# Kernel tuning notes

Measured on AMD Instinct MI355X. Metric: run time of the kernel, lower is better.

The kernel has to match this reference:

```python
import jax, jax.numpy as jnp
import numpy as np

BETA = 100.0
# (in_ch, out_ch) for the 12 effective 1x1-conv layers. ResNeXt blocks are
# fused: all branches read the same block input, so stacking branch weights
# along out-channels gives one GEMM per block.
LAYER_DIMS = [(259, 515), (515, 512), (512, 512), (512, 576), (576, 576),
              (576, 768), (768, 768), (768, 768), (768, 960), (960, 960),
              (960, 896), (896, 1)]


def setup_inputs() -> dict:
    key = jax.random.key(0)
    keys = jax.random.split(key, 2 + len(LAYER_DIMS))
    B, N = 2, 8192
    inp = {
        "input": jax.random.normal(keys[0], (B, N, 3), dtype=jnp.float32),
        "latent": jax.random.normal(keys[1], (B, 256), dtype=jnp.float32),
    }
    for i, (cin, cout) in enumerate(LAYER_DIMS):
        std = np.sqrt(2.0) / np.sqrt(cin)
        inp[f"W{i+1}"] = std * jax.random.normal(keys[2 + i], (cout, cin), dtype=jnp.float32)
        inp[f"b{i+1}"] = jnp.zeros((cout,), dtype=jnp.float32)
    return inp


def _sp(z):
    # torch Softplus(beta=100): softplus(beta*z)/beta (jax.nn.softplus is stable)
    return jax.nn.softplus(BETA * z) / BETA


def reference(input, latent,
              W1, b1, W2, b2, W3, b3, W4, b4, W5, b5, W6, b6,
              W7, b7, W8, b8, W9, b9, W10, b10, W11, b11, W12, b12):
    B, N, _ = input.shape
    lat = jnp.broadcast_to(latent[:, None, :], (B, N, latent.shape[-1]))
    x = jnp.concatenate([input, lat], axis=-1)  # (B, N, 259)
    input_con = x

    # layer 1: conv + softplus, grad seeded from first 3 input columns (xyz)
    z = x @ W1.T + b1                                   # (B, N, 515)
    g = jax.nn.sigmoid(BETA * z)[..., None] * W1[:, :3]  # (B, N, 515, 3)
    x = _sp(z)

    mids = [(W2, b2), (W3, b3), (W4, b4), (W5, b5), (W6, b6), (W7, b7),
            (W8, b8), (W9, b9), (W10, b10), (W11, b11)]
    for W, b in mids:  # fixed small layer loop (10 fused ResNeXt blocks)
        z = x @ W.T + b                                 # (B, N, Cout)
        g = jax.nn.sigmoid(BETA * z)[..., None] * jnp.einsum('oc,bnci->bnoi', W, g)
        x = _sp(z)

    # final 1x1 conv, no activation
    z = x @ W12.T + b12                                 # (B, N, 1)
    g = jnp.einsum('oc,bnci->bnoi', W12, g)             # (B, N, 1, 3)
    # torch returns conv output channel-first: (B, 1, N)
    return (z.transpose(0, 2, 1), g, input_con)
```

## Files before the change

### kernel.cpp

```cpp
#include <hip/hip_runtime.h>
#include <math.h>


typedef unsigned short u16;
typedef _Float16 f16;
typedef f16   f16x8  __attribute__((ext_vector_type(8)));
typedef float f32x16 __attribute__((ext_vector_type(16)));

__device__ __forceinline__ u16   f2h(float x){ return __builtin_bit_cast(u16, (f16)x); }
__device__ __forceinline__ float h2f(u16 b){ return (float)__builtin_bit_cast(f16, b); }

__device__ __forceinline__ void glld16(const void* g, void* l){
  __builtin_amdgcn_global_load_lds(
      (const __attribute__((address_space(1))) unsigned*)g,
      (__attribute__((address_space(3))) unsigned*)l, 16, 0, 0);
}

template<int N> __device__ __forceinline__ void wait_vmcnt(){
  static_assert(N == 0 || N == 6 || N == 9, "unsupported vmcnt literal");
  if constexpr (N == 0) asm volatile("s_waitcnt vmcnt(0)" ::: "memory");
  if constexpr (N == 6) asm volatile("s_waitcnt vmcnt(6)" ::: "memory");
  if constexpr (N == 9) asm volatile("s_waitcnt vmcnt(9)" ::: "memory");
}

template<int NP>
__global__ __launch_bounds__(256, 2)
void fused_layer(const u16* __restrict__ Sin, long long psIn, int kpad,
                 u16* __restrict__ Sout, long long psOut, int opitch,
                 const u16* __restrict__ Wh, const u16* __restrict__ Wl,
                 const float* __restrict__ bias, const float* __restrict__ Wfirst,
                 int cout, int cinFirst)
{
  constexpr bool FIRST = (NP == 2);
  constexpr int  S     = NP + 4;
  __shared__ u16 As[2][NP][4][64][8];
  __shared__ u16 Bs[2][2][4][128][8];

  int bx = blockIdx.x, by = blockIdx.y;
  {
    const int gx = gridDim.x, gy = gridDim.y;
    const int nwg = gx * gy;
    const int d   = by * gx + bx;
    if ((nwg & 7) == 0){
      const int q = nwg >> 3;
      const int t = (d & 7) * q + (d >> 3);
      by = t % gy;
      bx = t / gy;
    }
  }

  const int tid   = threadIdx.x;
  const int w     = tid >> 6;
  const int lane  = tid & 63;
  const int lrow  = lane & 31;
  const int lhalf = lane >> 5;
  const int mh    = w >> 1;
  const int oh    = w & 1;
  const int m0    = bx * 64;
  const int o0    = by * 128;

  f32x16 zinit = {};
  f32x16 accx[2];
  f32x16 accg[FIRST ? 1 : 3][2];
  accx[0] = zinit; accx[1] = zinit;
  if constexpr (!FIRST){
    #pragma unroll
    for (int j = 0; j < 3; ++j){ accg[j][0] = zinit; accg[j][1] = zinit; }
  }

  const u16* aSrc[NP];
  #pragma unroll
  for (int p = 0; p < NP; ++p)
    aSrc[p] = Sin + (long long)p * psIn + (long long)(m0 + lane) * kpad + w * 8;
  const u16* bSrc[2][2];
  #pragma unroll
  for (int h = 0; h < 2; ++h){
    const u16* Wx = h ? Wl : Wh;
    #pragma unroll
    for (int hf = 0; hf < 2; ++hf)
      bSrc[h][hf] = Wx + (long long)(o0 + hf*64 + lane) * kpad + w * 8;
  }

  auto stage = [&](int buf, int kElem){
    #pragma unroll
    for (int p = 0; p < NP; ++p)
      glld16(aSrc[p] + kElem, &As[buf][p][w][0][0]);
    #pragma unroll
    for (int h = 0; h < 2; ++h)
      #pragma unroll
      for (int hf = 0; hf < 2; ++hf)
        glld16(bSrc[h][hf] + kElem, &Bs[buf][h][w][hf*64][0]);
  };

  auto compute = [&](int buf){
    __builtin_amdgcn_s_setprio(1);
    #pragma unroll
    for (int s = 0; s < 2; ++s){
      const int kq = s*2 + lhalf;
      f16x8 a[NP];
      #pragma unroll
      for (int p = 0; p < NP; ++p)
        a[p] = *(const f16x8*)&As[buf][p][kq][mh*32 + lrow][0];
      #pragma unroll
      for (int f = 0; f < 2; ++f){
        const int oc = oh*64 + f*32 + lrow;
        f16x8 bh = *(const f16x8*)&Bs[buf][0][kq][oc][0];
        f16x8 bl = *(const f16x8*)&Bs[buf][1][kq][oc][0];
        accx[f] = __builtin_amdgcn_mfma_f32_32x32x16_f16(a[0], bh, accx[f], 0,0,0);
        accx[f] = __builtin_amdgcn_mfma_f32_32x32x16_f16(a[1], bh, accx[f], 0,0,0);
        accx[f] = __builtin_amdgcn_mfma_f32_32x32x16_f16(a[0], bl, accx[f], 0,0,0);
        if constexpr (!FIRST){
          #pragma unroll
          for (int j = 0; j < 3; ++j)
            accg[j][f] = __builtin_amdgcn_mfma_f32_32x32x16_f16(a[2+j], bh, accg[j][f], 0,0,0);
        }
      }
    }
    __builtin_amdgcn_s_setprio(0);
  };

  const int nk = kpad >> 5;
  stage(0, 0);
  stage(1, 32);
  int cur = 0;
  for (int t = 0; t < nk - 1; ++t){
    wait_vmcnt<S>();
    __builtin_amdgcn_s_barrier();
    compute(cur);
    asm volatile("s_waitcnt lgkmcnt(0)" ::: "memory");
    __builtin_amdgcn_s_barrier();
    if (t + 2 < nk) stage(cur, (t + 2) * 32);
    cur ^= 1;
  }
  wait_vmcnt<0>();
  __builtin_amdgcn_s_barrier();
  compute(cur);

  const int mb = m0 + mh*32;
  #pragma unroll
  for (int f = 0; f < 2; ++f){
    const int o = o0 + oh*64 + f*32 + lrow;
    if (o >= opitch) continue;
    const float bo = (o < cout) ? bias[o] : 0.f;
    float w0 = 0.f, w1 = 0.f, w2 = 0.f;
    if constexpr (FIRST){
      if (o < cout){
        w0 = Wfirst[(long long)o*cinFirst + 0];
        w1 = Wfirst[(long long)o*cinFirst + 1];
        w2 = Wfirst[(long long)o*cinFirst + 2];
      }
    }
    #pragma unroll
    for (int r = 0; r < 16; ++r){
      const int m = mb + (r & 3) + ((r >> 2) << 3) + (lhalf << 2);
      const float z    = accx[f][r] + bo;
      const float gate = 1.f / (1.f + expf(-100.f * z));
      const float sp   = fmaxf(z, 0.f) + 0.01f * log1pf(expf(-100.f * fabsf(z)));
      const long long idx = (long long)m * opitch + o;
      const u16 xh = f2h(sp);
      Sout[idx]          = xh;
      Sout[psOut + idx]  = f2h(sp - h2f(xh));
      if constexpr (FIRST){
        Sout[2*psOut + idx] = f2h(gate * w0);
        Sout[3*psOut + idx] = f2h(gate * w1);
        Sout[4*psOut + idx] = f2h(gate * w2);
      } else {
        Sout[2*psOut + idx] = f2h(gate * accg[0][f][r]);
        Sout[3*psOut + idx] = f2h(gate * accg[1][f][r]);
        Sout[4*psOut + idx] = f2h(gate * accg[2][f][r]);
      }
    }
  }
}

__global__ __launch_bounds__(256)
void final_layer(const u16* __restrict__ Sin, long long ps, int kpad,
                 const float* __restrict__ W, const float* __restrict__ bias,
                 float* __restrict__ out1, float* __restrict__ out2,
                 int cin, int mBase)
{
  const int lane = threadIdx.x & 63;
  const int wv   = threadIdx.x >> 6;
  const int m = blockIdx.x * 4 + wv;
  const u16* row = Sin + (long long)m * kpad;
  float s0=0.f, s1=0.f, s2=0.f, s3=0.f;
  for (int c = lane; c < cin; c += 64){
    const float w = W[c];
    s0 += (h2f(row[c]) + h2f(row[ps + c])) * w;
    s1 += h2f(row[2*ps + c]) * w;
    s2 += h2f(row[3*ps + c]) * w;
    s3 += h2f(row[4*ps + c]) * w;
  }
  #pragma unroll
  for (int off = 32; off > 0; off >>= 1){
    s0 += __shfl_xor(s0, off); s1 += __shfl_xor(s1, off);
    s2 += __shfl_xor(s2, off); s3 += __shfl_xor(s3, off);
  }
  if (lane == 0){
    out1[mBase + m] = s0 + bias[0];
    float* g = out2 + (long long)(mBase + m) * 3;
    g[0] = s1; g[1] = s2; g[2] = s3;
  }
}

__global__ void prep_input(const float* __restrict__ input,
                           const float* __restrict__ latent,
                           float* __restrict__ out3,
                           u16* __restrict__ x0, long long psX0, int N)
{
  const int m = blockIdx.x;
  const int b = m / N;
  const int c = threadIdx.x;
  if (c >= 288) return;
  float v = 0.f;
  if (c < 3) v = input[(long long)m*3 + c];
  else if (c < 259) v = latent[(long long)b*256 + (c - 3)];
  if (c < 259) out3[(long long)m*259 + c] = v;
  const u16 h = f2h(v);
  x0[(long long)m*288 + c]        = h;
  x0[psX0 + (long long)m*288 + c] = f2h(v - h2f(h));
}

__global__ void split_w(const float* __restrict__ W, u16* __restrict__ wh,
                        u16* __restrict__ wl, int cout, int cin, int kpad, int total)
{
  const int idx = blockIdx.x * 256 + threadIdx.x;
  if (idx >= total) return;
  const int o = idx / kpad, c = idx % kpad;
  const float v = (o < cout && c < cin) ? W[(long long)o*cin + c] : 0.f;
  const u16 h = f2h(v);
  wh[idx] = h;
  wl[idx] = f2h(v - h2f(h));
}

extern "C" void kernel_launch(void* const* d_in, const int* in_sizes, int n_in,
                              void* d_out, int out_size, void* d_ws, size_t ws_size,
                              hipStream_t stream)
{
  static const int CIN [12] = {259,515,512,512,576,576,768,768,768,960,960,896};
  static const int COUT[12] = {515,512,512,576,576,768,768,768,960,960,896,1};
  int NY[11], ROWS[11], KPAD[12];
  KPAD[0] = 288;
  for (int i = 0; i < 11; ++i){
    NY[i]    = (COUT[i] + 127) / 128;
    ROWS[i]  = NY[i] * 128;
    KPAD[i+1] = (COUT[i] + 31) & ~31;
  }

  const float* input  = (const float*)d_in[0];
  const float* latent = (const float*)d_in[1];
  auto Wp = [&](int i){ return (const float*)d_in[2 + 2*i]; };
  auto Bp = [&](int i){ return (const float*)d_in[3 + 2*i]; };

  const int Bn = in_sizes[1] / 256;
  const int Nn = in_sizes[0] / (3 * Bn);
  const int M  = Bn * Nn;

  float* out1 = (float*)d_out;
  float* out2 = out1 + M;
  float* out3 = out2 + (size_t)M * 3;

  char* wsp = (char*)d_ws;
  u16 *WH[11], *WL[11];
  for (int i = 0; i < 11; ++i){
    const size_t sz = (size_t)ROWS[i] * KPAD[i] * 2;
    WH[i] = (u16*)wsp; wsp += sz;
    WL[i] = (u16*)wsp; wsp += sz;
  }
  u16* x0 = (u16*)wsp;
  const long long psX0 = (long long)M * 288;
  wsp += (size_t)2 * psX0 * 2;

  const size_t used = (size_t)(wsp - (char*)d_ws);
  const size_t remain = (ws_size > used) ? (ws_size - used) : 0;
  const size_t perPoint = (size_t)2 * 5 * 960 * 2;
  long long pc = (long long)(remain / perPoint);
  pc &= ~63LL;
  int Pc = (int)((pc < (long long)M) ? pc : (long long)M);
  if (Pc < 64) Pc = 64;
  u16* bufA = (u16*)wsp;
  u16* bufB = bufA + (size_t)5 * Pc * 960;

  prep_input<<<M, 320, 0, stream>>>(input, latent, out3, x0, psX0, Nn);
  for (int i = 0; i < 11; ++i){
    const int total = ROWS[i] * KPAD[i];
    split_w<<<(total + 255)/256, 256, 0, stream>>>(
        Wp(i), WH[i], WL[i], COUT[i], CIN[i], KPAD[i], total);
  }

  for (int cm0 = 0; cm0 < M; cm0 += Pc){
    const int Mc = (M - cm0 < Pc) ? (M - cm0) : Pc;

    {
      dim3 g(Mc/64, NY[0]);
      fused_layer<2><<<g, 256, 0, stream>>>(
          x0 + (long long)cm0 * 288, psX0, 288,
          bufA, (long long)Pc * KPAD[1], KPAD[1],
          WH[0], WL[0], Bp(0), Wp(0), COUT[0], CIN[0]);
    }
    u16* src = bufA;
    u16* dst = bufB;
    for (int i = 1; i <= 10; ++i){
      dim3 g(Mc/64, NY[i]);
      fused_layer<5><<<g, 256, 0, stream>>>(
          src, (long long)Pc * KPAD[i], KPAD[i],
          dst, (long long)Pc * KPAD[i+1], KPAD[i+1],
          WH[i], WL[i], Bp(i), nullptr, COUT[i], 0);
      u16* t = src; src = dst; dst = t;
    }
    final_layer<<<Mc/4, 256, 0, stream>>>(
        src, (long long)Pc * KPAD[11], KPAD[11],
        Wp(11), Bp(11), out1, out2, CIN[11], cm0);
  }
}
```

Measured before the change: 2.646 ms.

## Replace forward-mode Jacobian propagation with stored gates and reverse-mode backward GEMMs

Forward-mode carried three gradient planes through every layer, adding three extra MFMA chains and three extra output planes per layer. The new version stores only each layer's sigmoid gate during the forward pass and then runs a reverse (vector-Jacobian) pass. That pass starts from W12 and multiplies by transposed weights, one plane per layer, and a final kernel contracts the result with W1[:, :3]. This removes about half the GEMM work but adds ten backward GEMM launches and keeps all eleven gate tensors in workspace, which can shrink the point chunk size.

Measured after the change: 2.705 ms. 1.02x slower.

```diff
diff --git a/kernel.cpp b/kernel.cpp
--- a/kernel.cpp
+++ b/kernel.cpp
@@ -17,37 +17,38 @@
 }
 
 template<int N> __device__ __forceinline__ void wait_vmcnt(){
-  static_assert(N == 0 || N == 6 || N == 9, "unsupported vmcnt literal");
+  static_assert(N == 0 || N == 3 || N == 6, "unsupported vmcnt literal");
   if constexpr (N == 0) asm volatile("s_waitcnt vmcnt(0)" ::: "memory");
+  if constexpr (N == 3) asm volatile("s_waitcnt vmcnt(3)" ::: "memory");
   if constexpr (N == 6) asm volatile("s_waitcnt vmcnt(6)" ::: "memory");
-  if constexpr (N == 9) asm volatile("s_waitcnt vmcnt(9)" ::: "memory");
-}
-
-template<int NP>
-__global__ __launch_bounds__(256, 2)
-void fused_layer(const u16* __restrict__ Sin, long long psIn, int kpad,
-                 u16* __restrict__ Sout, long long psOut, int opitch,
-                 const u16* __restrict__ Wh, const u16* __restrict__ Wl,
-                 const float* __restrict__ bias, const float* __restrict__ Wfirst,
-                 int cout, int cinFirst)
-{
-  constexpr bool FIRST = (NP == 2);
-  constexpr int  S     = NP + 4;
-  __shared__ u16 As[2][NP][4][64][8];
+}
+
+__device__ __forceinline__ void xcd_map(int& bx, int& by){
+  const int gx = gridDim.x, gy = gridDim.y;
+  const int nwg = gx * gy;
+  const int d   = by * gx + bx;
+  if ((nwg & 7) == 0){
+    const int q = nwg >> 3;
+    const int t = (d & 7) * q + (d >> 3);
+    by = t % gy;
+    bx = t / gy;
+  }
+}
+
+template<bool LAST>
+__global__ __launch_bounds__(256, 3)
+void fwd_layer(const u16* __restrict__ Sin, long long psIn, int kpad,
+               u16* __restrict__ SoutX, long long psOut,
+               u16* __restrict__ Gout, int opitch,
+               const u16* __restrict__ Wh, const u16* __restrict__ Wl,
+               const float* __restrict__ bias, const float* __restrict__ w12,
+               int cout)
+{
+  __shared__ u16 As[2][2][4][64][8];
   __shared__ u16 Bs[2][2][4][128][8];
 
   int bx = blockIdx.x, by = blockIdx.y;
-  {
-    const int gx = gridDim.x, gy = gridDim.y;
-    const int nwg = gx * gy;
-    const int d   = by * gx + bx;
-    if ((nwg & 7) == 0){
-      const int q = nwg >> 3;
-      const int t = (d & 7) * q + (d >> 3);
-      by = t % gy;
-      bx = t / gy;
-    }
-  }
+  xcd_map(bx, by);
 
   const int tid   = threadIdx.x;
   const int w     = tid >> 6;
@@ -61,16 +62,11 @@
 
   f32x16 zinit = {};
   f32x16 accx[2];
-  f32x16 accg[FIRST ? 1 : 3][2];
   accx[0] = zinit; accx[1] = zinit;
-  if constexpr (!FIRST){
-    #pragma unroll
-    for (int j = 0; j < 3; ++j){ accg[j][0] = zinit; accg[j][1] = zinit; }
-  }
-
-  const u16* aSrc[NP];
-  #pragma unroll
-  for (int p = 0; p < NP; ++p)
+
+  const u16* aSrc[2];
+  #pragma unroll
+  for (int p = 0; p < 2; ++p)
     aSrc[p] = Sin + (long long)p * psIn + (long long)(m0 + lane) * kpad + w * 8;
   const u16* bSrc[2][2];
   #pragma unroll
@@ -83,7 +79,7 @@
 
   auto stage = [&](int buf, int kElem){
     #pragma unroll
-    for (int p = 0; p < NP; ++p)
+    for (int p = 0; p < 2; ++p)
       glld16(aSrc[p] + kElem, &As[buf][p][w][0][0]);
     #pragma unroll
     for (int h = 0; h < 2; ++h)
@@ -97,23 +93,16 @@
     #pragma unroll
     for (int s = 0; s < 2; ++s){
       const int kq = s*2 + lhalf;
-      f16x8 a[NP];
-      #pragma unroll
-      for (int p = 0; p < NP; ++p)
-        a[p] = *(const f16x8*)&As[buf][p][kq][mh*32 + lrow][0];
+      f16x8 a0 = *(const f16x8*)&As[buf][0][kq][mh*32 + lrow][0];
+      f16x8 a1 = *(const f16x8*)&As[buf][1][kq][mh*32 + lrow][0];
       #pragma unroll
       for (int f = 0; f < 2; ++f){
         const int oc = oh*64 + f*32 + lrow;
         f16x8 bh = *(const f16x8*)&Bs[buf][0][kq][oc][0];
         f16x8 bl = *(const f16x8*)&Bs[buf][1][kq][oc][0];
-        accx[f] = __builtin_amdgcn_mfma_f32_32x32x16_f16(a[0], bh, accx[f], 0,0,0);
-        accx[f] = __builtin_amdgcn_mfma_f32_32x32x16_f16(a[1], bh, accx[f], 0,0,0);
-        accx[f] = __builtin_amdgcn_mfma_f32_32x32x16_f16(a[0], bl, accx[f], 0,0,0);
-        if constexpr (!FIRST){
-          #pragma unroll
-          for (int j = 0; j < 3; ++j)
-            accg[j][f] = __builtin_amdgcn_mfma_f32_32x32x16_f16(a[2+j], bh, accg[j][f], 0,0,0);
-        }
+        accx[f] = __builtin_amdgcn_mfma_f32_32x32x16_f16(a0, bh, accx[f], 0,0,0);
+        accx[f] = __builtin_amdgcn_mfma_f32_32x32x16_f16(a1, bh, accx[f], 0,0,0);
+        accx[f] = __builtin_amdgcn_mfma_f32_32x32x16_f16(a0, bl, accx[f], 0,0,0);
       }
     }
     __builtin_amdgcn_s_setprio(0);
@@ -124,7 +113,7 @@
   stage(1, 32);
   int cur = 0;
   for (int t = 0; t < nk - 1; ++t){
-    wait_vmcnt<S>();
+    wait_vmcnt<6>();
     __builtin_amdgcn_s_barrier();
     compute(cur);
     asm volatile("s_waitcnt lgkmcnt(0)" ::: "memory");
@@ -141,15 +130,9 @@
   for (int f = 0; f < 2; ++f){
     const int o = o0 + oh*64 + f*32 + lrow;
     if (o >= opitch) continue;
-    const float bo = (o < cout) ? bias[o] : 0.f;
-    float w0 = 0.f, w1 = 0.f, w2 = 0.f;
-    if constexpr (FIRST){
-      if (o < cout){
-        w0 = Wfirst[(long long)o*cinFirst + 0];
-        w1 = Wfirst[(long long)o*cinFirst + 1];
-        w2 = Wfirst[(long long)o*cinFirst + 2];
-      }
-    }
+    const bool real = (o < cout);
+    const float bo  = real ? bias[o] : 0.f;
+    const float wf  = (LAST && real) ? w12[o] : 0.f;
     #pragma unroll
     for (int r = 0; r < 16; ++r){
       const int m = mb + (r & 3) + ((r >> 2) << 3) + (lhalf << 2);
@@ -158,48 +141,140 @@
       const float sp   = fmaxf(z, 0.f) + 0.01f * log1pf(expf(-100.f * fabsf(z)));
       const long long idx = (long long)m * opitch + o;
       const u16 xh = f2h(sp);
-      Sout[idx]          = xh;
-      Sout[psOut + idx]  = f2h(sp - h2f(xh));
-      if constexpr (FIRST){
-        Sout[2*psOut + idx] = f2h(gate * w0);
-        Sout[3*psOut + idx] = f2h(gate * w1);
-        Sout[4*psOut + idx] = f2h(gate * w2);
-      } else {
-        Sout[2*psOut + idx] = f2h(gate * accg[0][f][r]);
-        Sout[3*psOut + idx] = f2h(gate * accg[1][f][r]);
-        Sout[4*psOut + idx] = f2h(gate * accg[2][f][r]);
+      SoutX[idx]         = xh;
+      SoutX[psOut + idx] = f2h(sp - h2f(xh));
+      float gv;
+      if (LAST) gv = gate * wf;
+      else      gv = real ? gate : 0.f;
+      Gout[idx] = f2h(gv);
+    }
+  }
+}
+
+__global__ __launch_bounds__(256, 4)
+void bwd_layer(const u16* __restrict__ Vin, int kpad,
+               u16* __restrict__ Vout, int opitch,
+               const u16* __restrict__ Gprev, const u16* __restrict__ Wt)
+{
+  __shared__ u16 As[2][4][64][8];
+  __shared__ u16 Bs[2][4][128][8];
+
+  int bx = blockIdx.x, by = blockIdx.y;
+  xcd_map(bx, by);
+
+  const int tid   = threadIdx.x;
+  const int w     = tid >> 6;
+  const int lane  = tid & 63;
+  const int lrow  = lane & 31;
+  const int lhalf = lane >> 5;
+  const int mh    = w >> 1;
+  const int oh    = w & 1;
+  const int m0    = bx * 64;
+  const int o0    = by * 128;
+
+  f32x16 zinit = {};
+  f32x16 acc[2];
+  acc[0] = zinit; acc[1] = zinit;
+
+  const u16* aSrc = Vin + (long long)(m0 + lane) * kpad + w * 8;
+  const u16* bSrc[2];
+  #pragma unroll
+  for (int hf = 0; hf < 2; ++hf)
+    bSrc[hf] = Wt + (long long)(o0 + hf*64 + lane) * kpad + w * 8;
+
+  auto stage = [&](int buf, int kElem){
+    glld16(aSrc + kElem, &As[buf][w][0][0]);
+    #pragma unroll
+    for (int hf = 0; hf < 2; ++hf)
+      glld16(bSrc[hf] + kElem, &Bs[buf][w][hf*64][0]);
+  };
+
+  auto compute = [&](int buf){
+    __builtin_amdgcn_s_setprio(1);
+    #pragma unroll
+    for (int s = 0; s < 2; ++s){
+      const int kq = s*2 + lhalf;
+      f16x8 a = *(const f16x8*)&As[buf][kq][mh*32 + lrow][0];
+      #pragma unroll
+      for (int f = 0; f < 2; ++f){
+        const int oc = oh*64 + f*32 + lrow;
+        f16x8 b = *(const f16x8*)&Bs[buf][kq][oc][0];
+        acc[f] = __builtin_amdgcn_mfma_f32_32x32x16_f16(a, b, acc[f], 0,0,0);
       }
     }
+    __builtin_amdgcn_s_setprio(0);
+  };
+
+  const int nk = kpad >> 5;
+  stage(0, 0);
+  stage(1, 32);
+  int cur = 0;
+  for (int t = 0; t < nk - 1; ++t){
+    wait_vmcnt<3>();
+    __builtin_amdgcn_s_barrier();
+    compute(cur);
+    asm volatile("s_waitcnt lgkmcnt(0)" ::: "memory");
+    __builtin_amdgcn_s_barrier();
+    if (t + 2 < nk) stage(cur, (t + 2) * 32);
+    cur ^= 1;
+  }
+  wait_vmcnt<0>();
+  __builtin_amdgcn_s_barrier();
+  compute(cur);
+
+  const int mb = m0 + mh*32;
+  #pragma unroll
+  for (int f = 0; f < 2; ++f){
+    const int o = o0 + oh*64 + f*32 + lrow;
+    if (o >= opitch) continue;
+    #pragma unroll
+    for (int r = 0; r < 16; ++r){
+      const int m = mb + (r & 3) + ((r >> 2) << 3) + (lhalf << 2);
+      const long long idx = (long long)m * opitch + o;
+      Vout[idx] = f2h(acc[f][r] * h2f(Gprev[idx]));
+    }
   }
 }
 
 __global__ __launch_bounds__(256)
-void final_layer(const u16* __restrict__ Sin, long long ps, int kpad,
-                 const float* __restrict__ W, const float* __restrict__ bias,
-                 float* __restrict__ out1, float* __restrict__ out2,
-                 int cin, int mBase)
+void final_z(const u16* __restrict__ Sx, long long ps, int kpad,
+             const float* __restrict__ W12, const float* __restrict__ b12,
+             float* __restrict__ out1, int cin, int mBase)
 {
   const int lane = threadIdx.x & 63;
   const int wv   = threadIdx.x >> 6;
   const int m = blockIdx.x * 4 + wv;
-  const u16* row = Sin + (long long)m * kpad;
-  float s0=0.f, s1=0.f, s2=0.f, s3=0.f;
-  for (int c = lane; c < cin; c += 64){
-    const float w = W[c];
-    s0 += (h2f(row[c]) + h2f(row[ps + c])) * w;
-    s1 += h2f(row[2*ps + c]) * w;
-    s2 += h2f(row[3*ps + c]) * w;
-    s3 += h2f(row[4*ps + c]) * w;
+  const u16* row = Sx + (long long)m * kpad;
+  float s = 0.f;
+  for (int c = lane; c < cin; c += 64)
+    s += (h2f(row[c]) + h2f(row[ps + c])) * W12[c];
+  #pragma unroll
+  for (int off = 32; off > 0; off >>= 1) s += __shfl_xor(s, off);
+  if (lane == 0) out1[mBase + m] = s + b12[0];
+}
+
+__global__ __launch_bounds__(256)
+void final_g(const u16* __restrict__ V0, int kpad,
+             const float* __restrict__ W1, int cinW,
+             float* __restrict__ out2, int width, int mBase)
+{
+  const int lane = threadIdx.x & 63;
+  const int wv   = threadIdx.x >> 6;
+  const int m = blockIdx.x * 4 + wv;
+  const u16* row = V0 + (long long)m * kpad;
+  float g0 = 0.f, g1 = 0.f, g2 = 0.f;
+  for (int o = lane; o < width; o += 64){
+    const float v = h2f(row[o]);
+    const float* wr = W1 + (long long)o * cinW;
+    g0 += v * wr[0]; g1 += v * wr[1]; g2 += v * wr[2];
   }
   #pragma unroll
   for (int off = 32; off > 0; off >>= 1){
-    s0 += __shfl_xor(s0, off); s1 += __shfl_xor(s1, off);
-    s2 += __shfl_xor(s2, off); s3 += __shfl_xor(s3, off);
+    g0 += __shfl_xor(g0, off); g1 += __shfl_xor(g1, off); g2 += __shfl_xor(g2, off);
   }
   if (lane == 0){
-    out1[mBase + m] = s0 + bias[0];
     float* g = out2 + (long long)(mBase + m) * 3;
-    g[0] = s1; g[1] = s2; g[2] = s3;
+    g[0] = g0; g[1] = g1; g[2] = g2;
   }
 }
 
@@ -233,24 +308,34 @@
   wl[idx] = f2h(v - h2f(h));
 }
 
+__global__ void split_wt(const float* __restrict__ W, u16* __restrict__ wt,
+                         int cout, int cin, int kpad, int total)
+{
+  const int idx = blockIdx.x * 256 + threadIdx.x;
+  if (idx >= total) return;
+  const int c = idx / kpad, k = idx % kpad;
+  const float v = (c < cin && k < cout) ? W[(long long)k*cin + c] : 0.f;
+  wt[idx] = f2h(v);
+}
+
 extern "C" void kernel_launch(void* const* d_in, const int* in_sizes, int n_in,
                               void* d_out, int out_size, void* d_ws, size_t ws_size,
                               hipStream_t stream)
 {
   static const int CIN [12] = {259,515,512,512,576,576,768,768,768,960,960,896};
   static const int COUT[12] = {515,512,512,576,576,768,768,768,960,960,896,1};
-  int NY[11], ROWS[11], KPAD[12];
-  KPAD[0] = 288;
-  for (int i = 0; i < 11; ++i){
-    NY[i]    = (COUT[i] + 127) / 128;
-    ROWS[i]  = NY[i] * 128;
-    KPAD[i+1] = (COUT[i] + 31) & ~31;
+  int PF[11], KPF[11], NYF[11], NYB[11];
+  for (int j = 0; j < 11; ++j){
+    PF[j]  = (COUT[j] + 31) & ~31;
+    KPF[j] = (j == 0) ? 288 : PF[j-1];
+    NYF[j] = (COUT[j] + 127) / 128;
+    NYB[j] = (CIN[j] + 127) / 128;
   }
 
   const float* input  = (const float*)d_in[0];
   const float* latent = (const float*)d_in[1];
-  auto Wp = [&](int i){ return (const float*)d_in[2 + 2*i]; };
-  auto Bp = [&](int i){ return (const float*)d_in[3 + 2*i]; };
+  auto Wp = [&](int j){ return (const float*)d_in[2 + 2*j]; };
+  auto Bp = [&](int j){ return (const float*)d_in[3 + 2*j]; };
 
   const int Bn = in_sizes[1] / 256;
   const int Nn = in_sizes[0] / (3 * Bn);
@@ -261,55 +346,86 @@
   float* out3 = out2 + (size_t)M * 3;
 
   char* wsp = (char*)d_ws;
-  u16 *WH[11], *WL[11];
-  for (int i = 0; i < 11; ++i){
-    const size_t sz = (size_t)ROWS[i] * KPAD[i] * 2;
-    WH[i] = (u16*)wsp; wsp += sz;
-    WL[i] = (u16*)wsp; wsp += sz;
+  u16 *WH[11], *WL[11], *WT[11];
+  for (int j = 0; j < 11; ++j){
+    const size_t sz = (size_t)NYF[j] * 128 * KPF[j] * 2;
+    WH[j] = (u16*)wsp; wsp += sz;
+    WL[j] = (u16*)wsp; wsp += sz;
+  }
+  for (int j = 1; j < 11; ++j){
+    const size_t sz = (size_t)NYB[j] * 128 * PF[j] * 2;
+    WT[j] = (u16*)wsp; wsp += sz;
   }
   u16* x0 = (u16*)wsp;
   const long long psX0 = (long long)M * 288;
   wsp += (size_t)2 * psX0 * 2;
 
-  const size_t used = (size_t)(wsp - (char*)d_ws);
+  size_t sumPF = 0;
+  for (int j = 0; j < 11; ++j) sumPF += (size_t)PF[j];
+  const size_t used   = (size_t)(wsp - (char*)d_ws);
   const size_t remain = (ws_size > used) ? (ws_size - used) : 0;
-  const size_t perPoint = (size_t)2 * 5 * 960 * 2;
+  const size_t perPoint = sumPF * 2 + (size_t)2 * 2 * 960 * 2;
   long long pc = (long long)(remain / perPoint);
   pc &= ~63LL;
   int Pc = (int)((pc < (long long)M) ? pc : (long long)M);
   if (Pc < 64) Pc = 64;
+
+  u16* gates[11];
+  for (int j = 0; j < 11; ++j){
+    gates[j] = (u16*)wsp; wsp += (size_t)Pc * PF[j] * 2;
+  }
   u16* bufA = (u16*)wsp;
-  u16* bufB = bufA + (size_t)5 * Pc * 960;
+  u16* bufB = bufA + (size_t)2 * Pc * 960;
+  u16* vA = bufB;
+  u16* vB = bufB + (size_t)Pc * 960;
 
   prep_input<<<M, 320, 0, stream>>>(input, latent, out3, x0, psX0, Nn);
-  for (int i = 0; i < 11; ++i){
-    const int total = ROWS[i] * KPAD[i];
+  for (int j = 0; j < 11; ++j){
+    const int total = NYF[j] * 128 * KPF[j];
     split_w<<<(total + 255)/256, 256, 0, stream>>>(
-        Wp(i), WH[i], WL[i], COUT[i], CIN[i], KPAD[i], total);
+        Wp(j), WH[j], WL[j], COUT[j], CIN[j], KPF[j], total);
+  }
+  for (int j = 1; j < 11; ++j){
+    const int total = NYB[j] * 128 * PF[j];
+    split_wt<<<(total + 255)/256, 256, 0, stream>>>(
+        Wp(j), WT[j], COUT[j], CIN[j], PF[j], total);
   }
 
   for (int cm0 = 0; cm0 < M; cm0 += Pc){
     const int Mc = (M - cm0 < Pc) ? (M - cm0) : Pc;
-
-    {
-      dim3 g(Mc/64, NY[0]);
-      fused_layer<2><<<g, 256, 0, stream>>>(
-          x0 + (long long)cm0 * 288, psX0, 288,
-          bufA, (long long)Pc * KPAD[1], KPAD[1],
-          WH[0], WL[0], Bp(0), Wp(0), COUT[0], CIN[0]);
-    }
-    u16* src = bufA;
-    u16* dst = bufB;
-    for (int i = 1; i <= 10; ++i){
-      dim3 g(Mc/64, NY[i]);
-      fused_layer<5><<<g, 256, 0, stream>>>(
-          src, (long long)Pc * KPAD[i], KPAD[i],
-          dst, (long long)Pc * KPAD[i+1], KPAD[i+1],
-          WH[i], WL[i], Bp(i), nullptr, COUT[i], 0);
-      u16* t = src; src = dst; dst = t;
-    }
-    final_layer<<<Mc/4, 256, 0, stream>>>(
-        src, (long long)Pc * KPAD[11], KPAD[11],
-        Wp(11), Bp(11), out1, out2, CIN[11], cm0);
-  }
-}
+    const int gx = Mc / 64;
+
+    u16* src = x0 + (long long)cm0 * 288;
+    long long psSrc = psX0;
+    int kp = 288;
+    u16* dstTbl[2] = { bufA, bufB };
+    for (int j = 0; j < 11; ++j){
+      u16* dst = dstTbl[j & 1];
+      dim3 g(gx, NYF[j]);
+      if (j == 10)
+        fwd_layer<true><<<g, 256, 0, stream>>>(
+            src, psSrc, kp, dst, (long long)Pc * PF[j], gates[j], PF[j],
+            WH[j], WL[j], Bp(j), Wp(11), COUT[j]);
+      else
+        fwd_layer<false><<<g, 256, 0, stream>>>(
+            src, psSrc, kp, dst, (long long)Pc * PF[j], gates[j], PF[j],
+            WH[j], WL[j], Bp(j), nullptr, COUT[j]);
+      src = dst; psSrc = (long long)Pc * PF[j]; kp = PF[j];
+    }
+
+    final_z<<<Mc/4, 256, 0, stream>>>(
+        src, psSrc, kp, Wp(11), Bp(11), out1, CIN[11], cm0);
+
+    u16* vin = gates[10];
+    for (int j = 10; j >= 1; --j){
+      u16* vout = (j & 1) ? vB : vA;
+      dim3 g(gx, NYB[j]);
+      bwd_layer<<<g, 256, 0, stream>>>(
+          vin, PF[j], vout, PF[j-1], gates[j-1], WT[j]);
+      vin = vout;
+    }
+
+    final_g<<<Mc/4, 256, 0, stream>>>(
+        vin, PF[0], Wp(0), CIN[0], out2, COUT[0], cm0);
+  }
+}
```
